# Kernel optimization log

Measured on AMD Instinct MI355X. Metric: run time of the kernel, lower is better.

## Reference

```python
import jax, jax.numpy as jnp
import numpy as np

HEADS, DIM_HEAD, LANDMARKS, PINV_ITERS, RES_K = 8, 64, 256, 6, 33
DIM = 512


def layer_norm(x, w, b, eps=1e-5):
    mu = x.mean(-1, keepdims=True)
    var = ((x - mu) ** 2).mean(-1, keepdims=True)
    return (x - mu) * jax.lax.rsqrt(var + eps) * w + b


def moore_penrose_pinv(x, iters=PINV_ITERS):
    # x: (b, h, m, m)
    abs_x = jnp.abs(x)
    col = abs_x.sum(-1)
    row = abs_x.sum(-2)
    z = jnp.swapaxes(x, -1, -2) / (jnp.max(col) * jnp.max(row))
    I = jnp.eye(x.shape[-1], dtype=x.dtype)
    for _ in range(iters):
        xz = x @ z
        z = 0.25 * z @ (13.0 * I - xz @ (15.0 * I - xz @ (7.0 * I - xz)))
    return z


def nystrom_attention(x, qkv_w, out_w, out_b, res_kernel):
    b, n, _ = x.shape
    h, dh, m = HEADS, DIM_HEAD, LANDMARKS
    l = n // m  # seq chosen divisible by landmarks
    qkv = x @ qkv_w  # (b, n, 3*h*dh)
    q, k, v = jnp.split(qkv, 3, axis=-1)
    def to_heads(t):
        return t.reshape(b, n, h, dh).transpose(0, 2, 1, 3)  # (b,h,n,dh)
    q, k, v = to_heads(q), to_heads(k), to_heads(v)
    q = q * (dh ** -0.5)
    # landmark pooling: mean over contiguous groups of size l
    q_l = q.reshape(b, h, m, l, dh).mean(axis=3)  # (b,h,m,dh)
    k_l = k.reshape(b, h, m, l, dh).mean(axis=3)
    attn1 = jax.nn.softmax(jnp.einsum('bhid,bhjd->bhij', q, k_l), axis=-1)   # (b,h,n,m)
    attn2 = jax.nn.softmax(jnp.einsum('bhid,bhjd->bhij', q_l, k_l), axis=-1) # (b,h,m,m)
    attn3 = jax.nn.softmax(jnp.einsum('bhid,bhjd->bhij', q_l, k), axis=-1)   # (b,h,m,n)
    attn2_inv = moore_penrose_pinv(attn2)
    out = (attn1 @ attn2_inv) @ (attn3 @ v)  # (b,h,n,dh)
    # depthwise residual conv over sequence dim, per head
    pad = (RES_K - 1) // 2
    out = out + jax.lax.conv_general_dilated(
        v, res_kernel, window_strides=(1, 1), padding=((pad, pad), (0, 0)),
        dimension_numbers=('NCHW', 'OIHW', 'NCHW'), feature_group_count=h)
    out = out.transpose(0, 2, 1, 3).reshape(b, n, h * dh)
    return out @ out_w + out_b


def trans_layer(x, p):
    return x + nystrom_attention(layer_norm(x, p['norm_w'], p['norm_b']),
                                 p['qkv_w'], p['out_w'], p['out_b'], p['res_k'])


def setup_inputs() -> dict:
    key = jax.random.key(0)
    ks = jax.random.split(key, 20)
    N, F = 16383, 1024
    d = {}
    d['x'] = jax.random.normal(ks[0], (1, N, F), dtype=jnp.float32)
    d['fc_w'] = jax.random.normal(ks[1], (F, DIM), dtype=jnp.float32) * 0.03
    d['fc_b'] = jnp.zeros((DIM,), dtype=jnp.float32)
    d['cls_token'] = jax.random.normal(ks[2], (1, 1, DIM), dtype=jnp.float32) * 1e-6
    for i, base in [(3, 'l1'), (9, 'l2')]:
        d[base + '_norm_w'] = jnp.ones((DIM,), dtype=jnp.float32)
        d[base + '_norm_b'] = jnp.zeros((DIM,), dtype=jnp.float32)
        d[base + '_qkv_w'] = jax.random.normal(ks[i], (DIM, 3 * DIM), dtype=jnp.float32) * 0.03
        d[base + '_out_w'] = jax.random.normal(ks[i + 1], (DIM, DIM), dtype=jnp.float32) * 0.03
        d[base + '_out_b'] = jnp.zeros((DIM,), dtype=jnp.float32)
        d[base + '_res_k'] = jax.random.normal(ks[i + 2], (HEADS, 1, RES_K, 1), dtype=jnp.float32) * 0.1
    d['norm_w'] = jnp.ones((DIM,), dtype=jnp.float32)
    d['norm_b'] = jnp.zeros((DIM,), dtype=jnp.float32)
    d['clf_w'] = jax.random.normal(ks[15], (DIM, 4), dtype=jnp.float32) * 0.05
    d['clf_b'] = jnp.zeros((4,), dtype=jnp.float32)
    return d


def reference(x, fc_w, fc_b, cls_token, l1_norm_w, l1_norm_b, l1_qkv_w, l1_out_w,
              l1_out_b, l1_res_k, l2_norm_w, l2_norm_b, l2_qkv_w, l2_out_w,
              l2_out_b, l2_res_k, norm_w, norm_b, clf_w, clf_b):
    h = jax.nn.relu(x @ fc_w + fc_b)                       # (1, N, 512)
    h = jnp.concatenate([cls_token, h], axis=1)            # (1, N+1, 512)
    p1 = dict(norm_w=l1_norm_w, norm_b=l1_norm_b, qkv_w=l1_qkv_w,
              out_w=l1_out_w, out_b=l1_out_b, res_k=l1_res_k)
    p2 = dict(norm_w=l2_norm_w, norm_b=l2_norm_b, qkv_w=l2_qkv_w,
              out_w=l2_out_w, out_b=l2_out_b, res_k=l2_res_k)
    h = trans_layer(h, p1)
    h = trans_layer(h, p2)
    h = layer_norm(h, norm_w, norm_b)[:, 0]                # (1, 512)
    logits = h @ clf_w + clf_b                             # (1, n_classes)
    hazards = jax.nn.sigmoid(logits)
    S = jnp.cumprod(1.0 - hazards, axis=1)
    return (hazards, S)
```

## Files before the change

### kernel.cpp

```cpp
#include <hip/hip_runtime.h>

#define NTOK 16384
#define NDIM 512
#define STP_LD 280

typedef __attribute__((ext_vector_type(8))) short short8;
typedef __attribute__((ext_vector_type(4))) float f32x4;

__device__ __forceinline__ unsigned short f2bf(float f) {
  unsigned u = __float_as_uint(f);
  u += 0x7fffu + ((u >> 16) & 1u);
  return (unsigned short)(u >> 16);
}
__device__ __forceinline__ float bf2f(unsigned short u) {
  return __uint_as_float((unsigned)u << 16);
}

__device__ __forceinline__ void gload_lds16(const void* g, void* l) {
  __builtin_amdgcn_global_load_lds(
      (const __attribute__((address_space(1))) unsigned int*)(unsigned long long)(g),
      (__attribute__((address_space(3))) unsigned int*)(unsigned long long)(l), 16, 0, 0);
}

template<int EPI>
__global__ __launch_bounds__(256) void gemm_bf16(
    const unsigned short* __restrict__ A, const unsigned short* __restrict__ Bt,
    float* __restrict__ C, const float* __restrict__ bias,
    int M, int N, int K, int Mstore)
{
  __shared__ unsigned short As[2][128 * 32];
  __shared__ unsigned short Bs[2][128 * 32];
  const int tid = threadIdx.x;
  const int id = blockIdx.y * gridDim.x + blockIdx.x;
  const int nwg8 = (gridDim.x * gridDim.y) >> 3;
  const int logical = (id & 7) * nwg8 + (id >> 3);
  const int row0 = (logical / gridDim.x) * 128;
  const int col0 = (logical % gridDim.x) * 128;
  const int wave = tid >> 6, lane = tid & 63;
  const int wm = (wave >> 1) * 64, wn = (wave & 1) * 64;
  const int quad = lane >> 4, m16 = lane & 15;

  const int r0 = tid >> 2;
  const int c8 = (tid & 3) * 8;
  const unsigned short* Ag0 = A + (size_t)(row0 + r0) * K + c8;
  const unsigned short* Ag1 = A + (size_t)(row0 + r0 + 64) * K + c8;
  const unsigned short* Bg0 = Bt + (size_t)(col0 + r0) * K + c8;
  const unsigned short* Bg1 = Bt + (size_t)(col0 + r0 + 64) * K + c8;
  char* AsB = (char*)As;
  char* BsB = (char*)Bs;
  const int wb = wave * 1024;

  f32x4 acc[4][4] = {};
  const int nc = K >> 5;
  gload_lds16(Ag0, AsB + wb);
  gload_lds16(Ag1, AsB + 4096 + wb);
  gload_lds16(Bg0, BsB + wb);
  gload_lds16(Bg1, BsB + 4096 + wb);
  __syncthreads();
  int b = 0;
  for (int c = 0; c < nc; c++) {
    if (c + 1 < nc) {
      int k1 = (c + 1) * 32;
      gload_lds16(Ag0 + k1, AsB + (b ^ 1) * 8192 + wb);
      gload_lds16(Ag1 + k1, AsB + (b ^ 1) * 8192 + 4096 + wb);
      gload_lds16(Bg0 + k1, BsB + (b ^ 1) * 8192 + wb);
      gload_lds16(Bg1 + k1, BsB + (b ^ 1) * 8192 + 4096 + wb);
    }
    short8 af[4], bf[4];
#pragma unroll
    for (int i = 0; i < 4; i++) {
      af[i] = *(const short8*)&As[b][(wm + i * 16 + m16) * 32 + quad * 8];
      bf[i] = *(const short8*)&Bs[b][(wn + i * 16 + m16) * 32 + quad * 8];
    }
#pragma unroll
    for (int i = 0; i < 4; i++)
#pragma unroll
      for (int j = 0; j < 4; j++)
        acc[i][j] = __builtin_amdgcn_mfma_f32_16x16x32_bf16(af[i], bf[j], acc[i][j], 0, 0, 0);
    __syncthreads();
    b ^= 1;
  }
#pragma unroll
  for (int i = 0; i < 4; i++) {
#pragma unroll
    for (int r = 0; r < 4; r++) {
      int gr = row0 + wm + i * 16 + quad * 4 + r;
      if (gr < Mstore) {
#pragma unroll
        for (int j = 0; j < 4; j++) {
          int gc = col0 + wn + j * 16 + m16;
          float v = acc[i][j][r];
          if (EPI == 1) { v += bias[gc]; v = fmaxf(v, 0.f); }
          if (EPI == 2) { v += bias[gc] + C[(size_t)gr * N + gc]; }
          C[(size_t)gr * N + gc] = v;
        }
      }
    }
  }
}

__global__ __launch_bounds__(256) void qkv_gemm(
    const unsigned short* __restrict__ A, const unsigned short* __restrict__ Bt,
    unsigned short* __restrict__ qb, unsigned short* __restrict__ kb,
    unsigned short* __restrict__ vTb,
    float* __restrict__ q_l, float* __restrict__ k_lT,
    unsigned short* __restrict__ q_lb, unsigned short* __restrict__ k_lb)
{
  __shared__ unsigned short As[2][128 * 32];
  __shared__ unsigned short Bs[2][128 * 32];
  __shared__ unsigned short vt[128 * 136];
  const int tid = threadIdx.x;
  const int id = blockIdx.y * gridDim.x + blockIdx.x;
  const int nwg8 = (gridDim.x * gridDim.y) >> 3;
  const int logical = (id & 7) * nwg8 + (id >> 3);
  const int bx = logical % 12, by = logical / 12;
  const int row0 = by * 128, col0 = bx * 128;
  const int wave = tid >> 6, lane = tid & 63;
  const int wm = (wave >> 1) * 64, wn = (wave & 1) * 64;
  const int quad = lane >> 4, m16 = lane & 15;

  const int r0 = tid >> 2;
  const int c8 = (tid & 3) * 8;
  const unsigned short* Ag0 = A + (size_t)(row0 + r0) * 512 + c8;
  const unsigned short* Ag1 = A + (size_t)(row0 + r0 + 64) * 512 + c8;
  const unsigned short* Bg0 = Bt + (size_t)(col0 + r0) * 512 + c8;
  const unsigned short* Bg1 = Bt + (size_t)(col0 + r0 + 64) * 512 + c8;
  char* AsB = (char*)As;
  char* BsB = (char*)Bs;
  const int wb = wave * 1024;

  f32x4 acc[4][4] = {};
  gload_lds16(Ag0, AsB + wb);
  gload_lds16(Ag1, AsB + 4096 + wb);
  gload_lds16(Bg0, BsB + wb);
  gload_lds16(Bg1, BsB + 4096 + wb);
  __syncthreads();
  int b = 0;
  for (int c = 0; c < 16; c++) {
    if (c < 15) {
      int k1 = (c + 1) * 32;
      gload_lds16(Ag0 + k1, AsB + (b ^ 1) * 8192 + wb);
      gload_lds16(Ag1 + k1, AsB + (b ^ 1) * 8192 + 4096 + wb);
      gload_lds16(Bg0 + k1, BsB + (b ^ 1) * 8192 + wb);
      gload_lds16(Bg1 + k1, BsB + (b ^ 1) * 8192 + 4096 + wb);
    }
    short8 af[4], bf[4];
#pragma unroll
    for (int i = 0; i < 4; i++) {
      af[i] = *(const short8*)&As[b][(wm + i * 16 + m16) * 32 + quad * 8];
      bf[i] = *(const short8*)&Bs[b][(wn + i * 16 + m16) * 32 + quad * 8];
    }
#pragma unroll
    for (int i = 0; i < 4; i++)
#pragma unroll
      for (int j = 0; j < 4; j++)
        acc[i][j] = __builtin_amdgcn_mfma_f32_16x16x32_bf16(af[i], bf[j], acc[i][j], 0, 0, 0);
    __syncthreads();
    b ^= 1;
  }

  const int sel = bx >> 2;
  if (sel == 2) {
#pragma unroll
    for (int i = 0; i < 4; i++)
#pragma unroll
      for (int j = 0; j < 4; j++) {
        int c_l = wn + j * 16 + m16;
        int r_b = wm + i * 16 + quad * 4;
        ushort4 o;
        o.x = f2bf(acc[i][j][0]); o.y = f2bf(acc[i][j][1]);
        o.z = f2bf(acc[i][j][2]); o.w = f2bf(acc[i][j][3]);
        *(ushort4*)&vt[c_l * 136 + r_b] = o;
      }
    __syncthreads();
    const int gc0 = col0 - 1024;
    const int u = tid & 15, cc = tid >> 4;
#pragma unroll
    for (int pass = 0; pass < 8; pass++) {
      int c = pass * 16 + cc;
      short8 v8 = *(const short8*)&vt[c * 136 + u * 8];
      *(short8*)(vTb + (size_t)(gc0 + c) * NTOK + row0 + u * 8) = v8;
    }
  } else {
    const bool isq = (sel == 0);
#pragma unroll
    for (int i = 0; i < 4; i++)
#pragma unroll
      for (int r = 0; r < 4; r++) {
        int gr = row0 + wm + i * 16 + quad * 4 + r;
#pragma unroll
        for (int j = 0; j < 4; j++) {
          int gc = col0 + wn + j * 16 + m16;
          float v = acc[i][j][r];
          if (isq) qb[(size_t)gr * 512 + gc] = f2bf(v * 0.125f);
          else     kb[(size_t)gr * 512 + (gc - 512)] = f2bf(v);
        }
      }
    float ps[4];
#pragma unroll
    for (int j = 0; j < 4; j++) {
      float s = 0.f;
#pragma unroll
      for (int i = 0; i < 4; i++)
#pragma unroll
        for (int r = 0; r < 4; r++) s += acc[i][j][r];
      s += __shfl_xor(s, 16);
      s += __shfl_xor(s, 32);
      ps[j] = s;
    }
    if (quad == 0) {
      const int jg = by * 2 + (wm >> 6);
      const float sc = isq ? (0.125f / 64.f) : (1.f / 64.f);
#pragma unroll
      for (int j = 0; j < 4; j++) {
        int gc = col0 + wn + j * 16 + m16 - (isq ? 0 : 512);
        int hh = gc >> 6, d = gc & 63;
        float p = ps[j] * sc;
        if (isq) {
          size_t o = ((size_t)(hh * 256 + jg)) * 64 + d;
          q_l[o] = p;
          q_lb[o] = f2bf(p);
        } else {
          k_lT[((size_t)hh * 64 + d) * 256 + jg] = p;
          size_t of = ((size_t)hh << 14) + (jg >> 6) * 4096 + (d >> 5) * 2048
                    + ((jg >> 4) & 3) * 512 + ((d >> 3) & 3) * 128 + (jg & 15) * 8 + (d & 7);
          k_lb[of] = f2bf(p);
        }
      }
    }
  }
}

template<bool WN, bool WT, bool WF>
__global__ __launch_bounds__(256) void bmm_pinv64(
    const unsigned short* __restrict__ A, const unsigned short* __restrict__ Bt,
    unsigned short* __restrict__ Cn, unsigned short* __restrict__ Ct,
    float* __restrict__ Cf,
    float an, float bn, float at, float bt)
{
  const int hh = blockIdx.z;
  A  += (size_t)hh << 16;
  Bt += (size_t)hh << 16;
  __shared__ unsigned short As[2][64 * 32];
  __shared__ unsigned short Bs[2][64 * 32];
  const int tid = threadIdx.x;
  const int row0 = blockIdx.y * 64, col0 = blockIdx.x * 64;
  const int wave = tid >> 6, lane = tid & 63;
  const int wm = (wave >> 1) * 32, wn = (wave & 1) * 32;
  const int quad = lane >> 4, m16 = lane & 15;
  const int sr = wave * 16 + (lane >> 2);
  const int sc = (lane & 3) * 8;
  const unsigned short* Ag = A + (size_t)(row0 + sr) * 256 + sc;
  const unsigned short* Bg = Bt + (size_t)(col0 + sr) * 256 + sc;
  char* AsW = (char*)As + wave * 1024;
  char* BsW = (char*)Bs + wave * 1024;

  f32x4 acc[2][2] = {};
  gload_lds16(Ag, AsW);
  gload_lds16(Bg, BsW);
  __syncthreads();
  int b = 0;
  for (int c = 0; c < 8; c++) {
    if (c < 7) {
      gload_lds16(Ag + (c + 1) * 32, AsW + (b ^ 1) * 4096);
      gload_lds16(Bg + (c + 1) * 32, BsW + (b ^ 1) * 4096);
    }
    short8 af[2], bfr[2];
#pragma unroll
    for (int i = 0; i < 2; i++) {
      af[i]  = *(const short8*)&As[b][(wm + i * 16 + m16) * 32 + quad * 8];
      bfr[i] = *(const short8*)&Bs[b][(wn + i * 16 + m16) * 32 + quad * 8];
    }
#pragma unroll
    for (int i = 0; i < 2; i++)
#pragma unroll
      for (int j = 0; j < 2; j++)
        acc[i][j] = __builtin_amdgcn_mfma_f32_16x16x32_bf16(af[i], bfr[j], acc[i][j], 0, 0, 0);
    __syncthreads();
    b ^= 1;
  }
  unsigned short* CnH = Cn + ((size_t)hh << 16);
  unsigned short* CtH = Ct + ((size_t)hh << 16);
  float* CfH = WF ? (Cf + ((size_t)hh << 16)) : nullptr;
#pragma unroll
  for (int i = 0; i < 2; i++) {
#pragma unroll
    for (int r = 0; r < 4; r++) {
      int gr = row0 + wm + i * 16 + quad * 4 + r;
#pragma unroll
      for (int j = 0; j < 2; j++) {
        int gc = col0 + wn + j * 16 + m16;
        float p = acc[i][j][r];
        float diag = (gr == gc) ? 1.f : 0.f;
        if (WN) {
          unsigned short nb_ = f2bf(an * p + bn * diag);
          CnH[(size_t)gr * 256 + gc] = nb_;
          if (WF) CfH[(size_t)gr * 256 + gc] = bf2f(nb_);
        }
        if (WT) CtH[(size_t)gc * 256 + gr] = f2bf(at * p + bt * diag);
      }
    }
  }
}

__global__ void castpad_x(const float* __restrict__ x, unsigned short* __restrict__ xb,
                          size_t nvalid) {
  size_t i4 = ((size_t)blockIdx.x * 256 + threadIdx.x) * 4;
  float4 v = make_float4(0.f, 0.f, 0.f, 0.f);
  if (i4 < nvalid) v = *(const float4*)(x + i4);
  ushort4 o;
  o.x = f2bf(v.x); o.y = f2bf(v.y); o.z = f2bf(v.z); o.w = f2bf(v.w);
  *(ushort4*)(xb + i4) = o;
}

__global__ __launch_bounds__(256) void transpose_cast(
    const float* __restrict__ in, unsigned short* __restrict__ out, int R, int C)
{
  __shared__ float tile[32][33];
  int r0 = blockIdx.x * 32, c0 = blockIdx.y * 32;
  int tx = threadIdx.x & 31, ty = threadIdx.x >> 5;
  for (int yy = ty; yy < 32; yy += 8)
    tile[yy][tx] = in[(size_t)(r0 + yy) * C + c0 + tx];
  __syncthreads();
  for (int yy = ty; yy < 32; yy += 8)
    out[(size_t)(c0 + yy) * R + r0 + tx] = f2bf(tile[tx][yy]);
}

__global__ __launch_bounds__(256) void conv_seq(
    const unsigned short* __restrict__ vTb, const float* __restrict__ res_k,
    unsigned short* __restrict__ convT)
{
  const int c = blockIdx.y;
  const int h = c >> 6;
  const int i0 = (blockIdx.x * 256 + threadIdx.x) * 8;
  float rk[33];
#pragma unroll
  for (int u = 0; u < 33; u++) rk[u] = res_k[h * 33 + u];
  const unsigned short* vr = vTb + (size_t)c * NTOK;
  float win[40];
#pragma unroll
  for (int ch = 0; ch < 5; ch++) {
    int a = i0 - 16 + ch * 8;
    if (a >= 0 && a < NTOK) {
      ushort4 u0 = *(const ushort4*)(vr + a);
      ushort4 u1 = *(const ushort4*)(vr + a + 4);
      win[ch * 8 + 0] = bf2f(u0.x); win[ch * 8 + 1] = bf2f(u0.y);
      win[ch * 8 + 2] = bf2f(u0.z); win[ch * 8 + 3] = bf2f(u0.w);
      win[ch * 8 + 4] = bf2f(u1.x); win[ch * 8 + 5] = bf2f(u1.y);
      win[ch * 8 + 6] = bf2f(u1.z); win[ch * 8 + 7] = bf2f(u1.w);
    } else {
#pragma unroll
      for (int u = 0; u < 8; u++) win[ch * 8 + u] = 0.f;
    }
  }
  ushort4 o0, o1;
  float out[8];
#pragma unroll
  for (int jj = 0; jj < 8; jj++) {
    float s = 0.f;
#pragma unroll
    for (int u = 0; u < 33; u++) s += rk[u] * win[jj + u];
    out[jj] = s;
  }
  o0.x = f2bf(out[0]); o0.y = f2bf(out[1]); o0.z = f2bf(out[2]); o0.w = f2bf(out[3]);
  o1.x = f2bf(out[4]); o1.y = f2bf(out[5]); o1.z = f2bf(out[6]); o1.w = f2bf(out[7]);
  *(ushort4*)(convT + (size_t)c * NTOK + i0) = o0;
  *(ushort4*)(convT + (size_t)c * NTOK + i0 + 4) = o1;
}

template<bool W2>
__global__ __launch_bounds__(256) void bmm_f32(
    const float* __restrict__ A, const float* __restrict__ B, float* __restrict__ C,
    float* __restrict__ C2, int M, int N, int K, float alpha, float beta, float gamma)
{
  const int h = blockIdx.z;
  A += (size_t)h * M * K; B += (size_t)h * K * N;
  size_t cb = (size_t)h * M * N;
  __shared__ float As[16][64];
  __shared__ float Bs[16][64];
  const int tid = threadIdx.x;
  const int row0 = blockIdx.y * 64, col0 = blockIdx.x * 64;
  const int ty = tid >> 4, tx = tid & 15;
  const int ar = tid >> 2, ac = (tid & 3) << 2;
  const int bk = tid >> 4, bj = (tid & 15) << 2;
  float acc[4][4] = {};
  float4 a  = *(const float4*)(A + (size_t)(row0 + ar) * K + ac);
  float4 bv = *(const float4*)(B + (size_t)bk * N + col0 + bj);
  for (int k0 = 0; k0 < K; k0 += 16) {
    As[ac + 0][ar] = a.x; As[ac + 1][ar] = a.y; As[ac + 2][ar] = a.z; As[ac + 3][ar] = a.w;
    *(float4*)&Bs[bk][bj] = bv;
    __syncthreads();
    if (k0 + 16 < K) {
      a  = *(const float4*)(A + (size_t)(row0 + ar) * K + k0 + 16 + ac);
      bv = *(const float4*)(B + (size_t)(k0 + 16 + bk) * N + col0 + bj);
    }
#pragma unroll
    for (int kk = 0; kk < 16; kk++) {
      float4 av = *(float4*)&As[kk][ty << 2];
      float4 bvv = *(float4*)&Bs[kk][tx << 2];
      float a4[4] = {av.x, av.y, av.z, av.w};
      float b4[4] = {bvv.x, bvv.y, bvv.z, bvv.w};
#pragma unroll
      for (int ii = 0; ii < 4; ii++)
#pragma unroll
        for (int jj = 0; jj < 4; jj++) acc[ii][jj] += a4[ii] * b4[jj];
    }
    __syncthreads();
  }
#pragma unroll
  for (int ii = 0; ii < 4; ii++) {
    int gr = row0 + (ty << 2) + ii;
#pragma unroll
    for (int jj = 0; jj < 4; jj++) {
      int gc = col0 + (tx << 2) + jj;
      float diag = (gr == gc) ? 1.f : 0.f;
      float v = alpha * acc[ii][jj] + beta * diag;
      C[cb + (size_t)gr * N + gc] = v;
      if (W2) C2[cb + (size_t)gr * N + gc] = gamma * diag - v;
    }
  }
}

__global__ void cls_copy(const float* __restrict__ cls, float* __restrict__ h) {
  int t = threadIdx.x;
  if (t < 512) h[t] = cls[t];
}

__global__ __launch_bounds__(256) void layernorm_rows(
    const float* __restrict__ x, unsigned short* __restrict__ y,
    const float* __restrict__ w, const float* __restrict__ b)
{
  const int row = blockIdx.x, tid = threadIdx.x;
  const float* xr = x + (size_t)row * NDIM;
  float2 v = ((const float2*)xr)[tid];
  float sum = v.x + v.y, sq = v.x * v.x + v.y * v.y;
#pragma unroll
  for (int off = 32; off; off >>= 1) { sum += __shfl_xor(sum, off); sq += __shfl_xor(sq, off); }
  __shared__ float r1[4], r2[4];
  if ((tid & 63) == 0) { r1[tid >> 6] = sum; r2[tid >> 6] = sq; }
  __syncthreads();
  sum = r1[0] + r1[1] + r1[2] + r1[3];
  sq  = r2[0] + r2[1] + r2[2] + r2[3];
  float mu = sum * (1.f / 512.f);
  float var = sq * (1.f / 512.f) - mu * mu;
  float rs = rsqrtf(var + 1e-5f);
  float a = (v.x - mu) * rs * w[2 * tid]     + b[2 * tid];
  float c = (v.y - mu) * rs * w[2 * tid + 1] + b[2 * tid + 1];
  ((unsigned*)(y + (size_t)row * NDIM))[tid] = (unsigned)f2bf(a) | ((unsigned)f2bf(c) << 16);
}

__global__ __launch_bounds__(256) void attn2_softmax(
    const float* __restrict__ q_l, const float* __restrict__ k_lT,
    float* __restrict__ x2, unsigned short* __restrict__ x2b)
{
  int row = blockIdx.x, h = blockIdx.y, j = threadIdx.x;
  __shared__ float qrow[64];
  __shared__ float red[4];
  if (j < 64) qrow[j] = q_l[(size_t)(h * 256 + row) * 64 + j];
  __syncthreads();
  const float* kt = k_lT + ((size_t)h * 64) * 256 + j;
  float s = 0.f;
#pragma unroll 8
  for (int d = 0; d < 64; d++) s += qrow[d] * kt[(size_t)d * 256];
  float m = s;
#pragma unroll
  for (int off = 32; off; off >>= 1) m = fmaxf(m, __shfl_xor(m, off));
  if ((j & 63) == 0) red[j >> 6] = m;
  __syncthreads();
  m = fmaxf(fmaxf(red[0], red[1]), fmaxf(red[2], red[3]));
  __syncthreads();
  float e = __expf(s - m), l = e;
#pragma unroll
  for (int off = 32; off; off >>= 1) l += __shfl_xor(l, off);
  if ((j & 63) == 0) red[j >> 6] = l;
  __syncthreads();
  l = red[0] + red[1] + red[2] + red[3];
  float val = e / l;
  size_t o = ((size_t)(h * 256 + row) << 8) + j;
  x2[o] = val;
  x2b[o] = f2bf(val);
}

__global__ __launch_bounds__(256) void colrow_max(const float* __restrict__ x2,
                                                  float* __restrict__ scal)
{
  const int h = blockIdx.x, tid = threadIdx.x;
  const float* xh = x2 + ((size_t)h << 16);
  float mx = -1e30f;
  if (blockIdx.y == 0) {
    const int wave = tid >> 6, lane = tid & 63;
    for (int r = wave; r < 256; r += 4) {
      float4 v = *(const float4*)(xh + (size_t)r * 256 + lane * 4);
      float s = v.x + v.y + v.z + v.w;
#pragma unroll
      for (int off = 32; off; off >>= 1) s += __shfl_xor(s, off);
      mx = fmaxf(mx, s);
    }
  } else {
    float cs = 0.f;
    for (int r0 = 0; r0 < 256; r0 += 8) {
      float v[8];
#pragma unroll
      for (int u = 0; u < 8; u++) v[u] = xh[(size_t)(r0 + u) * 256 + tid];
#pragma unroll
      for (int u = 0; u < 8; u++) cs += v[u];
    }
    mx = cs;
  }
#pragma unroll
  for (int off = 32; off; off >>= 1) mx = fmaxf(mx, __shfl_xor(mx, off));
  __shared__ float red[4];
  if ((tid & 63) == 0) red[tid >> 6] = mx;
  __syncthreads();
  if (tid == 0) {
    float m = fmaxf(fmaxf(red[0], red[1]), fmaxf(red[2], red[3]));
    atomicMax((unsigned int*)&scal[blockIdx.y], __float_as_uint(m));
  }
}

__global__ void zinit_bf(const float* __restrict__ x2, unsigned short* __restrict__ zb,
                         unsigned short* __restrict__ zTb, const float* __restrict__ scal)
{
  int idx = blockIdx.x * 256 + threadIdx.x;
  int hh = idx >> 16, i = (idx >> 8) & 255, j = idx & 255;
  float den = scal[0] * scal[1];
  float val = x2[idx] / den;
  unsigned short b = f2bf(val);
  zTb[idx] = b;
  zb[(hh << 16) + (j << 8) + i] = b;
}

__global__ __launch_bounds__(256) void flash_fused(
    const unsigned short* __restrict__ q_lb, const unsigned short* __restrict__ kb,
    const unsigned short* __restrict__ vTb,
    float* __restrict__ Opart, float* __restrict__ mlpart)
{
  const int ks = blockIdx.x, qg = blockIdx.y, h = blockIdx.z;
  const int tid = threadIdx.x;
  const int wave = tid >> 6, lane = tid & 63;
  const int quad = lane >> 4, m16 = lane & 15;

  __shared__ unsigned short Ks[2][4096];
  __shared__ unsigned short Vs[2][4096];
  __shared__ unsigned short pbuf_all[4][16 * 72];
  unsigned short* pbuf = pbuf_all[wave];

  const int key00 = ks * 512;

  const int sr  = (wave << 3) + (lane >> 3);
  const int sxz = (lane & 7) ^ ((lane >> 3) & 7);
  const unsigned short* kst0 = kb + (size_t)(key00 + sr) * 512 + (h << 6) + sxz * 8;
  const unsigned short* kst1 = kst0 + (size_t)32 * 512;
  const unsigned short* vst0 = vTb + (size_t)((h << 6) + sr) * NTOK + key00 + sxz * 8;
  const unsigned short* vst1 = vst0 + (size_t)32 * NTOK;
  char* ldsKw = (char*)&Ks[0][0] + (wave << 10);
  char* ldsVw = (char*)&Vs[0][0] + (wave << 10);

  const int xs  = m16 & 7;
  const int co0 = ((quad) ^ xs) << 3;
  const int co1 = ((4 + quad) ^ xs) << 3;

  const int qrow_w = qg * 64 + wave * 16;
  const unsigned short* qbase = q_lb + ((size_t)h << 14) + (size_t)(qrow_w + m16) * 64;
  short8 aq0 = *(const short8*)(qbase + quad * 8);
  short8 aq1 = *(const short8*)(qbase + 32 + quad * 8);

  float m_e[4], l_e[4];
#pragma unroll
  for (int e = 0; e < 4; e++) { m_e[e] = -1e30f; l_e[e] = 0.f; }
  f32x4 acc_o[4] = {};

#define FF_STAGE(bb, cc) do {                                   \
    size_t ko = (size_t)(cc) * 32768; int vo = (cc) * 64;       \
    gload_lds16(kst0 + ko, ldsKw + (bb) * 8192);                \
    gload_lds16(kst1 + ko, ldsKw + (bb) * 8192 + 4096);         \
    gload_lds16(vst0 + vo, ldsVw + (bb) * 8192);                \
    gload_lds16(vst1 + vo, ldsVw + (bb) * 8192 + 4096);         \
  } while (0)

  FF_STAGE(0, 0);
  __syncthreads();
  int b = 0;
  for (int c = 0; c < 8; c++) {
    if (c < 7) FF_STAGE(b ^ 1, c + 1);
    const unsigned short* Kb = Ks[b];
    const unsigned short* Vb = Vs[b];
    f32x4 s[4] = {};
    __builtin_amdgcn_s_setprio(1);
#pragma unroll
    for (int kt = 0; kt < 4; kt++) {
      const unsigned short* krow = Kb + ((kt << 4) + m16) * 64;
      short8 b0 = *(const short8*)(krow + co0);
      short8 b1 = *(const short8*)(krow + co1);
      s[kt] = __builtin_amdgcn_mfma_f32_16x16x32_bf16(aq0, b0, s[kt], 0, 0, 0);
      s[kt] = __builtin_amdgcn_mfma_f32_16x16x32_bf16(aq1, b1, s[kt], 0, 0, 0);
    }
    __builtin_amdgcn_s_setprio(0);
#pragma unroll
    for (int e = 0; e < 4; e++) {
      float mx = fmaxf(fmaxf(s[0][e], s[1][e]), fmaxf(s[2][e], s[3][e]));
      mx = fmaxf(mx, __shfl_xor(mx, 1));
      mx = fmaxf(mx, __shfl_xor(mx, 2));
      mx = fmaxf(mx, __shfl_xor(mx, 4));
      mx = fmaxf(mx, __shfl_xor(mx, 8));
      float mn = fmaxf(m_e[e], mx);
      float scale = __expf(m_e[e] - mn);
      m_e[e] = mn;
      float sum = 0.f;
#pragma unroll
      for (int kt = 0; kt < 4; kt++) {
        float ev = __expf(s[kt][e] - mn);
        s[kt][e] = ev;
        sum += ev;
      }
      sum += __shfl_xor(sum, 1); sum += __shfl_xor(sum, 2);
      sum += __shfl_xor(sum, 4); sum += __shfl_xor(sum, 8);
      l_e[e] = l_e[e] * scale + sum;
#pragma unroll
      for (int dt = 0; dt < 4; dt++) acc_o[dt][e] *= scale;
    }
#pragma unroll
    for (int kt = 0; kt < 4; kt++)
#pragma unroll
      for (int e = 0; e < 4; e++)
        pbuf[(quad * 4 + e) * 72 + kt * 16 + m16] = f2bf(s[kt][e]);
    asm volatile("s_waitcnt lgkmcnt(0)" ::: "memory");
    short8 ap0 = *(const short8*)&pbuf[m16 * 72 + quad * 8];
    short8 ap1 = *(const short8*)&pbuf[m16 * 72 + 32 + quad * 8];
    __builtin_amdgcn_s_setprio(1);
#pragma unroll
    for (int dt = 0; dt < 4; dt++) {
      const unsigned short* vrow = Vb + ((dt << 4) + m16) * 64;
      short8 bv0 = *(const short8*)(vrow + co0);
      short8 bv1 = *(const short8*)(vrow + co1);
      acc_o[dt] = __builtin_amdgcn_mfma_f32_16x16x32_bf16(ap0, bv0, acc_o[dt], 0, 0, 0);
      acc_o[dt] = __builtin_amdgcn_mfma_f32_16x16x32_bf16(ap1, bv1, acc_o[dt], 0, 0, 0);
    }
    __builtin_amdgcn_s_setprio(0);
    __syncthreads();
    b ^= 1;
  }
#undef FF_STAGE
  float* ob = Opart + ((size_t)(ks * 8 + h) * 256 + qrow_w) * 64;
#pragma unroll
  for (int dt = 0; dt < 4; dt++)
#pragma unroll
    for (int e = 0; e < 4; e++)
      ob[(size_t)(quad * 4 + e) * 64 + dt * 16 + m16] = acc_o[dt][e];
  if (m16 == 0) {
    float* mlb = mlpart + ((size_t)(ks * 8 + h) * 256 + qrow_w) * 2;
#pragma unroll
    for (int e = 0; e < 4; e++) {
      mlb[(quad * 4 + e) * 2]     = m_e[e];
      mlb[(quad * 4 + e) * 2 + 1] = l_e[e];
    }
  }
}

__global__ __launch_bounds__(256) void flash_merge(
    const float* __restrict__ Opart, const float* __restrict__ mlpart,
    float* __restrict__ kv)
{
  const int rc = blockIdx.x, h = blockIdx.y, tid = threadIdx.x;
  const int r = rc * 32 + (tid >> 3);
  const int d0 = (tid & 7) * 8;
  float M = -1e30f;
  for (int ks = 0; ks < 32; ks++)
    M = fmaxf(M, mlpart[((size_t)(ks * 8 + h) * 256 + r) * 2]);
  float L = 0.f;
  float o[8];
#pragma unroll
  for (int j = 0; j < 8; j++) o[j] = 0.f;
  for (int ks = 0; ks < 32; ks++) {
    const float* mlb = mlpart + ((size_t)(ks * 8 + h) * 256 + r) * 2;
    float w = __expf(mlb[0] - M);
    L += mlb[1] * w;
    const float* op = Opart + ((size_t)(ks * 8 + h) * 256 + r) * 64 + d0;
    float4 a = *(const float4*)op;
    float4 b = *(const float4*)(op + 4);
    o[0] += a.x * w; o[1] += a.y * w; o[2] += a.z * w; o[3] += a.w * w;
    o[4] += b.x * w; o[5] += b.y * w; o[6] += b.z * w; o[7] += b.w * w;
  }
  float invL = 1.f / L;
  float* out = kv + ((size_t)(h * 256 + r)) * 64 + d0;
#pragma unroll
  for (int j = 0; j < 8; j++) out[j] = o[j] * invL;
}

__global__ __launch_bounds__(256) void bmt_kernel(
    const float* __restrict__ zf, const float* __restrict__ kv,
    unsigned short* __restrict__ BmT)
{
  const int jb = blockIdx.x, hh = blockIdx.y, tid = threadIdx.x;
  __shared__ float zt[64 * 256];
  const float* zsrc = zf + ((size_t)hh << 16) + (size_t)(jb * 64) * 256;
  for (int rep = 0; rep < 16; rep++) {
    int e4 = (rep * 256 + tid) * 4;
    *(float4*)&zt[e4] = *(const float4*)(zsrc + e4);
  }
  __syncthreads();
  const int d = tid & 63, jg = tid >> 6;
  const float* kvh = kv + ((size_t)hh << 14) + d;
  float acc[16];
#pragma unroll
  for (int u = 0; u < 16; u++) acc[u] = 0.f;
  for (int k0 = 0; k0 < 256; k0 += 8) {
    float kv8[8];
#pragma unroll
    for (int u = 0; u < 8; u++) kv8[u] = kvh[(size_t)(k0 + u) << 6];
#pragma unroll
    for (int jj = 0; jj < 16; jj++) {
      const float* zr = &zt[(jg * 16 + jj) * 256 + k0];
#pragma unroll
      for (int u = 0; u < 8; u++) acc[jj] += zr[u] * kv8[u];
    }
  }
  unsigned short* obh = BmT + ((size_t)hh << 14) + (d >> 5) * 8192
                        + ((d >> 4) & 1) * 512 + (d & 15) * 8;
#pragma unroll
  for (int jj = 0; jj < 16; jj++) {
    int j = jb * 64 + jg * 16 + jj;
    obh[(j >> 5) * 1024 + ((j >> 3) & 3) * 128 + (j & 7)] = f2bf(acc[jj]);
  }
}

__global__ __launch_bounds__(256) void attn1_out(
    const unsigned short* __restrict__ qb, const unsigned short* __restrict__ k_lb,
    const unsigned short* __restrict__ BmT, const unsigned short* __restrict__ convT,
    unsigned short* __restrict__ attn_out)
{
  const int qc = blockIdx.x, h = blockIdx.y, tid = threadIdx.x;
  const int q0 = qc * 32;
  const int wave = tid >> 6, lane = tid & 63;
  const int quad = lane >> 4, m16 = lane & 15;

  __shared__ unsigned short stp[32 * STP_LD];
  __shared__ float redm[4][32], redl[4][32];

  const int mi3 = (wave & 1) * 16;
  const int nbase = (wave >> 1) * 32;
  const int gi0 = q0 + mi3 + quad * 4;
  ushort4 cv4_[2];
#pragma unroll
  for (int t = 0; t < 2; t++) {
    int d = nbase + t * 16 + m16;
    cv4_[t] = *(const ushort4*)(convT + (size_t)((h << 6) + d) * NTOK + gi0);
  }

  f32x4 acc1[2][4] = {};
  {
    const unsigned short* qbase = qb + (size_t)q0 * 512 + (h << 6);
    const unsigned short* kf = k_lb + ((size_t)h << 14) + (wave << 12);
#pragma unroll
    for (int kc = 0; kc < 2; kc++) {
      short8 aq[2], bk[4];
#pragma unroll
      for (int i = 0; i < 2; i++)
        aq[i] = *(const short8*)(qbase + (size_t)(i * 16 + m16) * 512 + kc * 32 + quad * 8);
#pragma unroll
      for (int n = 0; n < 4; n++)
        bk[n] = *(const short8*)(kf + kc * 2048 + n * 512 + lane * 8);
#pragma unroll
      for (int i = 0; i < 2; i++)
#pragma unroll
        for (int n = 0; n < 4; n++)
          acc1[i][n] = __builtin_amdgcn_mfma_f32_16x16x32_bf16(aq[i], bk[n], acc1[i][n], 0, 0, 0);
    }
  }
#pragma unroll
  for (int i = 0; i < 2; i++) {
#pragma unroll
    for (int e = 0; e < 4; e++) {
      float mx = fmaxf(fmaxf(acc1[i][0][e], acc1[i][1][e]), fmaxf(acc1[i][2][e], acc1[i][3][e]));
      mx = fmaxf(mx, __shfl_xor(mx, 1));
      mx = fmaxf(mx, __shfl_xor(mx, 2));
      mx = fmaxf(mx, __shfl_xor(mx, 4));
      mx = fmaxf(mx, __shfl_xor(mx, 8));
      if (m16 == 0) redm[wave][i * 16 + quad * 4 + e] = mx;
    }
  }
  __syncthreads();
#pragma unroll
  for (int i = 0; i < 2; i++) {
#pragma unroll
    for (int e = 0; e < 4; e++) {
      int r = i * 16 + quad * 4 + e;
      float gm = fmaxf(fmaxf(redm[0][r], redm[1][r]), fmaxf(redm[2][r], redm[3][r]));
      float s = 0.f;
#pragma unroll
      for (int n = 0; n < 4; n++) {
        float ev = __expf(acc1[i][n][e] - gm);
        acc1[i][n][e] = ev;
        s += ev;
      }
      s += __shfl_xor(s, 1); s += __shfl_xor(s, 2);
      s += __shfl_xor(s, 4); s += __shfl_xor(s, 8);
      if (m16 == 0) redl[wave][r] = s;
    }
  }
#pragma unroll
  for (int i = 0; i < 2; i++)
#pragma unroll
    for (int n = 0; n < 4; n++) {
      int col = wave * 64 + n * 16 + m16;
#pragma unroll
      for (int e = 0; e < 4; e++)
        stp[(i * 16 + quad * 4 + e) * STP_LD + col] = f2bf(acc1[i][n][e]);
    }
  __syncthreads();

  f32x4 acc3[2] = {};
  {
    const unsigned short* bf_ = BmT + ((size_t)h << 14) + ((nbase >> 5) << 13);
#pragma unroll
    for (int kc = 0; kc < 8; kc++) {
      short8 ap = *(const short8*)&stp[(mi3 + m16) * STP_LD + kc * 32 + quad * 8];
#pragma unroll
      for (int t = 0; t < 2; t++) {
        short8 bp = *(const short8*)(bf_ + kc * 1024 + t * 512 + lane * 8);
        acc3[t] = __builtin_amdgcn_mfma_f32_16x16x32_bf16(ap, bp, acc3[t], 0, 0, 0);
      }
    }
  }
#pragma unroll
  for (int t = 0; t < 2; t++) {
    int d = nbase + t * 16 + m16;
    unsigned short cvs[4] = {cv4_[t].x, cv4_[t].y, cv4_[t].z, cv4_[t].w};
#pragma unroll
    for (int e = 0; e < 4; e++) {
      int lr = mi3 + quad * 4 + e;
      float l = redl[0][lr] + redl[1][lr] + redl[2][lr] + redl[3][lr];
      float v = acc3[t][e] / l + bf2f(cvs[e]);
      attn_out[((size_t)(gi0 + e) << 9) + (h << 6) + d] = f2bf(v);
    }
  }
}

__global__ __launch_bounds__(256) void final_head(
    const float* __restrict__ hrow, const float* __restrict__ nw, const float* __restrict__ nb,
    const float* __restrict__ cw, const float* __restrict__ cb, float* __restrict__ out)
{
  const int tid = threadIdx.x;
  __shared__ float ln0[512];
  __shared__ float r1[4], r2[4];
  __shared__ float lg[4][4];
  float2 v = ((const float2*)hrow)[tid];
  float sum = v.x + v.y, sq = v.x * v.x + v.y * v.y;
#pragma unroll
  for (int off = 32; off; off >>= 1) { sum += __shfl_xor(sum, off); sq += __shfl_xor(sq, off); }
  if ((tid & 63) == 0) { r1[tid >> 6] = sum; r2[tid >> 6] = sq; }
  __syncthreads();
  sum = r1[0] + r1[1] + r1[2] + r1[3];
  sq  = r2[0] + r2[1] + r2[2] + r2[3];
  float mu = sum * (1.f / 512.f);
  float var = sq * (1.f / 512.f) - mu * mu;
  float rs = rsqrtf(var + 1e-5f);
  ln0[2 * tid]     = (v.x - mu) * rs * nw[2 * tid]     + nb[2 * tid];
  ln0[2 * tid + 1] = (v.y - mu) * rs * nw[2 * tid + 1] + nb[2 * tid + 1];
  __syncthreads();
  float p[4] = {0.f, 0.f, 0.f, 0.f};
  for (int k = tid; k < 512; k += 256) {
    float lv = ln0[k];
#pragma unroll
    for (int c = 0; c < 4; c++) p[c] += lv * cw[k * 4 + c];
  }
#pragma unroll
  for (int off = 32; off; off >>= 1)
#pragma unroll
    for (int c = 0; c < 4; c++) p[c] += __shfl_xor(p[c], off);
  if ((tid & 63) == 0) {
    int w = tid >> 6;
#pragma unroll
    for (int c = 0; c < 4; c++) lg[w][c] = p[c];
  }
  __syncthreads();
  if (tid == 0) {
    float cum = 1.f;
    for (int c = 0; c < 4; c++) {
      float logit = lg[0][c] + lg[1][c] + lg[2][c] + lg[3][c] + cb[c];
      float hz = 1.f / (1.f + __expf(-logit));
      out[c] = hz;
      cum *= (1.f - hz);
      out[4 + c] = cum;
    }
  }
}

extern "C" void kernel_launch(void* const* d_in, const int* in_sizes, int n_in,
                              void* d_out, int out_size, void* d_ws, size_t ws_size,
                              hipStream_t stream)
{
  (void)in_sizes; (void)n_in; (void)out_size; (void)ws_size;
  const float* x    = (const float*)d_in[0];
  const float* fc_w = (const float*)d_in[1];
  const float* fc_b = (const float*)d_in[2];
  const float* cls  = (const float*)d_in[3];
  const float* nw[2]   = {(const float*)d_in[4],  (const float*)d_in[10]};
  const float* nb[2]   = {(const float*)d_in[5],  (const float*)d_in[11]};
  const float* qkvw[2] = {(const float*)d_in[6],  (const float*)d_in[12]};
  const float* outw[2] = {(const float*)d_in[7],  (const float*)d_in[13]};
  const float* outb[2] = {(const float*)d_in[8],  (const float*)d_in[14]};
  const float* resk[2] = {(const float*)d_in[9],  (const float*)d_in[15]};
  const float* fnw = (const float*)d_in[16];
  const float* fnb = (const float*)d_in[17];
  const float* cw  = (const float*)d_in[18];
  const float* cb  = (const float*)d_in[19];

  float* ws = (float*)d_ws;
  float* h    = ws; ws += (size_t)NTOK * NDIM;
  float* qkv  = ws; ws += (size_t)NTOK * 1536;
  float* bigv = ws; ws += (size_t)(512 * NTOK) / 2;
  float* q_l  = ws; ws += 8 * 256 * 64;
  float* k_lT = ws; ws += 8 * 256 * 64;
  float* x2   = ws; ws += 8 * 256 * 256;
  float* zf   = ws; ws += 8 * 256 * 256;
  float* zfin = ws; ws += 8 * 256 * 256;
  float* tA   = ws; ws += 8 * 256 * 256;
  float* tB   = ws; ws += 8 * 256 * 256;
  float* tC   = ws; ws += 8 * 256 * 256;
  float* kv   = ws; ws += 8 * 256 * 64;
  float* scal = ws; ws += 64;
  unsigned short* actb = (unsigned short*)ws; ws += (size_t)NTOK * NDIM / 2;
  unsigned short* wT   = (unsigned short*)ws; ws += (1536 * 512) / 2;
  unsigned short* qb   = (unsigned short*)ws; ws += (size_t)NTOK * NDIM / 2;
  unsigned short* k_lb = (unsigned short*)ws; ws += (8 * 256 * 64) / 2;
  unsigned short* q_lb = (unsigned short*)ws; ws += (8 * 256 * 64) / 2;
  unsigned short* x2b  = (unsigned short*)ws; ws += (8 * 256 * 256) / 2;
  unsigned short* zb0  = (unsigned short*)ws; ws += (8 * 256 * 256) / 2;
  unsigned short* zb1  = (unsigned short*)ws; ws += (8 * 256 * 256) / 2;
  unsigned short* zT0  = (unsigned short*)ws; ws += (8 * 256 * 256) / 2;
  unsigned short* zT1  = (unsigned short*)ws; ws += (8 * 256 * 256) / 2;
  unsigned short* xzb  = (unsigned short*)ws; ws += (8 * 256 * 256) / 2;
  unsigned short* t1T  = (unsigned short*)ws; ws += (8 * 256 * 256) / 2;
  unsigned short* t2T  = (unsigned short*)ws; ws += (8 * 256 * 256) / 2;
  unsigned short* t3T  = (unsigned short*)ws; ws += (8 * 256 * 256) / 2;
  unsigned short* BmT  = (unsigned short*)ws; ws += (8 * 64 * 256) / 2;
  unsigned short* kbuf = (unsigned short*)ws; ws += (size_t)NTOK * NDIM / 2;

  unsigned short* xb  = (unsigned short*)qkv;
  unsigned short* vTb = (unsigned short*)bigv;
  float* Opart  = qkv;
  float* mlpart = qkv + (size_t)32 * 8 * 256 * 64;
  unsigned short* convT = (unsigned short*)(qkv + (size_t)32 * 8 * 256 * 64 + 32 * 8 * 256 * 2);

  unsigned short* zbp[2] = {zb0, zb1};
  unsigned short* zTp[2] = {zT0, zT1};

  castpad_x<<<16384, 256, 0, stream>>>(x, xb, (size_t)16383 * 1024);
  transpose_cast<<<dim3(32, 16), 256, 0, stream>>>(fc_w, wT, 1024, 512);
  gemm_bf16<1><<<dim3(4, 128), 256, 0, stream>>>(xb, wT, h + 512, fc_b,
                                                 16384, 512, 1024, 16383);
  cls_copy<<<1, 512, 0, stream>>>(cls, h);

  for (int L = 0; L < 2; L++) {
    layernorm_rows<<<NTOK, 256, 0, stream>>>(h, actb, nw[L], nb[L]);
    transpose_cast<<<dim3(16, 48), 256, 0, stream>>>(qkvw[L], wT, 512, 1536);
    qkv_gemm<<<dim3(12, 128), 256, 0, stream>>>(actb, wT, qb, kbuf, vTb,
                                                q_l, k_lT, q_lb, k_lb);
    attn2_softmax<<<dim3(256, 8), 256, 0, stream>>>(q_l, k_lT, x2, x2b);
    hipMemsetAsync(scal, 0, 2 * sizeof(float), stream);
    colrow_max<<<dim3(8, 2), 256, 0, stream>>>(x2, scal);
    zinit_bf<<<2048, 256, 0, stream>>>(x2, zbp[0], zTp[0], scal);

    flash_fused<<<dim3(32, 4, 8), 256, 0, stream>>>(q_lb, kbuf, vTb, Opart, mlpart);
    flash_merge<<<dim3(8, 8), 256, 0, stream>>>(Opart, mlpart, kv);
    conv_seq<<<dim3(8, 512), 256, 0, stream>>>(vTb, resk[L], convT);

    int cur = 0;
    dim3 pg(4, 4, 8);
    for (int it = 0; it < 5; it++) {
      bmm_pinv64<true,  true, false><<<pg, 256, 0, stream>>>(x2b, zTp[cur], xzb, t1T, nullptr,
                                                             1.f, 0.f, -1.f, 7.f);
      bmm_pinv64<false, true, false><<<pg, 256, 0, stream>>>(xzb, t1T, nullptr, t2T, nullptr,
                                                             0.f, 0.f, -1.f, 15.f);
      bmm_pinv64<false, true, false><<<pg, 256, 0, stream>>>(xzb, t2T, nullptr, t3T, nullptr,
                                                             0.f, 0.f, -1.f, 13.f);
      if (it < 4)
        bmm_pinv64<true, true, false><<<pg, 256, 0, stream>>>(zbp[cur], t3T, zbp[cur ^ 1],
                                                              zTp[cur ^ 1], nullptr,
                                                              0.25f, 0.f, 0.25f, 0.f);
      else
        bmm_pinv64<true, true, true><<<pg, 256, 0, stream>>>(zbp[cur], t3T, zbp[cur ^ 1],
                                                             zTp[cur ^ 1], zf,
                                                             0.25f, 0.f, 0.25f, 0.f);
      cur ^= 1;
    }
    bmm_f32<true ><<<dim3(4, 4, 8), 256, 0, stream>>>(x2, zf, tA, tB, 256, 256, 256, 1.f, 0.f, 7.f);
    bmm_f32<false><<<dim3(4, 4, 8), 256, 0, stream>>>(tA, tB, tC, nullptr, 256, 256, 256, -1.f, 15.f, 0.f);
    bmm_f32<false><<<dim3(4, 4, 8), 256, 0, stream>>>(tA, tC, tB, nullptr, 256, 256, 256, -1.f, 13.f, 0.f);
    bmm_f32<false><<<dim3(4, 4, 8), 256, 0, stream>>>(zf, tB, zfin, nullptr, 256, 256, 256, 0.25f, 0.f, 0.f);

    bmt_kernel<<<dim3(4, 8), 256, 0, stream>>>(zfin, kv, BmT);
    attn1_out<<<dim3(512, 8), 256, 0, stream>>>(qb, k_lb, BmT, convT, actb);
    transpose_cast<<<dim3(16, 16), 256, 0, stream>>>(outw[L], wT, 512, 512);
    gemm_bf16<2><<<dim3(4, 128), 256, 0, stream>>>(actb, wT, h, outb[L],
                                                   NTOK, 512, 512, NTOK);
  }
  final_head<<<1, 256, 0, stream>>>(h, fnw, fnb, cw, cb, (float*)d_out);
}
```

Baseline: 951.1 us.

## Stage QKV epilogue through aliased LDS and drop the memset and cls launches

The q/k epilogue of qkv_gemm now writes bf16 results into a shared-memory tile and stores rows back as coalesced 16-byte vectors, replacing scattered 2-byte global stores. The staging tile is aliased onto the double-buffered A/B operand buffers, which shrinks the LDS footprint and may allow more resident workgroups. The cls row copy is folded into castpad_x. The atomicMax with its preceding memset is replaced by per-block partial maxima that zinit_bf reduces, removing two small launches per layer. This adds a block barrier in the epilogue and requires scal to hold 16 floats.

```diff
diff --git a/kernel.cpp b/kernel.cpp
--- a/kernel.cpp
+++ b/kernel.cpp
@@ -106,9 +106,10 @@
     float* __restrict__ q_l, float* __restrict__ k_lT,
     unsigned short* __restrict__ q_lb, unsigned short* __restrict__ k_lb)
 {
-  __shared__ unsigned short As[2][128 * 32];
-  __shared__ unsigned short Bs[2][128 * 32];
-  __shared__ unsigned short vt[128 * 136];
+  __shared__ unsigned short smem[17408];
+  unsigned short* AsU = smem;
+  unsigned short* BsU = smem + 8192;
+  unsigned short* vt  = smem;
   const int tid = threadIdx.x;
   const int id = blockIdx.y * gridDim.x + blockIdx.x;
   const int nwg8 = (gridDim.x * gridDim.y) >> 3;
@@ -125,8 +126,8 @@
   const unsigned short* Ag1 = A + (size_t)(row0 + r0 + 64) * 512 + c8;
   const unsigned short* Bg0 = Bt + (size_t)(col0 + r0) * 512 + c8;
   const unsigned short* Bg1 = Bt + (size_t)(col0 + r0 + 64) * 512 + c8;
-  char* AsB = (char*)As;
-  char* BsB = (char*)Bs;
+  char* AsB = (char*)AsU;
+  char* BsB = (char*)BsU;
   const int wb = wave * 1024;
 
   f32x4 acc[4][4] = {};
@@ -147,8 +148,8 @@
     short8 af[4], bf[4];
 #pragma unroll
     for (int i = 0; i < 4; i++) {
-      af[i] = *(const short8*)&As[b][(wm + i * 16 + m16) * 32 + quad * 8];
-      bf[i] = *(const short8*)&Bs[b][(wn + i * 16 + m16) * 32 + quad * 8];
+      af[i] = *(const short8*)&AsU[b * 4096 + (wm + i * 16 + m16) * 32 + quad * 8];
+      bf[i] = *(const short8*)&BsU[b * 4096 + (wn + i * 16 + m16) * 32 + quad * 8];
     }
 #pragma unroll
     for (int i = 0; i < 4; i++)
@@ -183,17 +184,16 @@
     }
   } else {
     const bool isq = (sel == 0);
+    const float mul = isq ? 0.125f : 1.f;
 #pragma unroll
     for (int i = 0; i < 4; i++)
 #pragma unroll
-      for (int r = 0; r < 4; r++) {
-        int gr = row0 + wm + i * 16 + quad * 4 + r;
-#pragma unroll
-        for (int j = 0; j < 4; j++) {
-          int gc = col0 + wn + j * 16 + m16;
-          float v = acc[i][j][r];
-          if (isq) qb[(size_t)gr * 512 + gc] = f2bf(v * 0.125f);
-          else     kb[(size_t)gr * 512 + (gc - 512)] = f2bf(v);
+      for (int j = 0; j < 4; j++) {
+        int lc = wn + j * 16 + m16;
+#pragma unroll
+        for (int r = 0; r < 4; r++) {
+          int lr = wm + i * 16 + quad * 4 + r;
+          vt[lr * 136 + lc] = f2bf(acc[i][j][r] * mul);
         }
       }
     float ps[4];
@@ -227,6 +227,16 @@
           k_lb[of] = f2bf(p);
         }
       }
+    }
+    __syncthreads();
+    unsigned short* ob = isq ? (qb + (size_t)row0 * 512 + col0)
+                             : (kb + (size_t)row0 * 512 + (col0 - 512));
+    const int u = tid & 15, cc = tid >> 4;
+#pragma unroll
+    for (int pass = 0; pass < 8; pass++) {
+      int rloc = pass * 16 + cc;
+      short8 v8 = *(const short8*)&vt[rloc * 136 + u * 8];
+      *(short8*)(ob + (size_t)rloc * 512 + u * 8) = v8;
     }
   }
 }
@@ -304,13 +314,16 @@
 }
 
 __global__ void castpad_x(const float* __restrict__ x, unsigned short* __restrict__ xb,
-                          size_t nvalid) {
+                          size_t nvalid, const float* __restrict__ cls,
+                          float* __restrict__ h) {
   size_t i4 = ((size_t)blockIdx.x * 256 + threadIdx.x) * 4;
   float4 v = make_float4(0.f, 0.f, 0.f, 0.f);
   if (i4 < nvalid) v = *(const float4*)(x + i4);
   ushort4 o;
   o.x = f2bf(v.x); o.y = f2bf(v.y); o.z = f2bf(v.z); o.w = f2bf(v.w);
   *(ushort4*)(xb + i4) = o;
+  if (blockIdx.x == 0 && threadIdx.x < 128)
+    *(float4*)(h + threadIdx.x * 4) = *(const float4*)(cls + threadIdx.x * 4);
 }
 
 __global__ __launch_bounds__(256) void transpose_cast(
@@ -421,11 +434,6 @@
   }
 }
 
-__global__ void cls_copy(const float* __restrict__ cls, float* __restrict__ h) {
-  int t = threadIdx.x;
-  if (t < 512) h[t] = cls[t];
-}
-
 __global__ __launch_bounds__(256) void layernorm_rows(
     const float* __restrict__ x, unsigned short* __restrict__ y,
     const float* __restrict__ w, const float* __restrict__ b)
@@ -512,10 +520,8 @@
   __shared__ float red[4];
   if ((tid & 63) == 0) red[tid >> 6] = mx;
   __syncthreads();
-  if (tid == 0) {
-    float m = fmaxf(fmaxf(red[0], red[1]), fmaxf(red[2], red[3]));
-    atomicMax((unsigned int*)&scal[blockIdx.y], __float_as_uint(m));
-  }
+  if (tid == 0)
+    scal[blockIdx.y * 8 + h] = fmaxf(fmaxf(red[0], red[1]), fmaxf(red[2], red[3]));
 }
 
 __global__ void zinit_bf(const float* __restrict__ x2, unsigned short* __restrict__ zb,
@@ -523,7 +529,10 @@
 {
   int idx = blockIdx.x * 256 + threadIdx.x;
   int hh = idx >> 16, i = (idx >> 8) & 255, j = idx & 255;
-  float den = scal[0] * scal[1];
+  float m0 = scal[0], m1 = scal[8];
+#pragma unroll
+  for (int u = 1; u < 8; u++) { m0 = fmaxf(m0, scal[u]); m1 = fmaxf(m1, scal[8 + u]); }
+  float den = m0 * m1;
   float val = x2[idx] / den;
   unsigned short b = f2bf(val);
   zTb[idx] = b;
@@ -946,11 +955,10 @@
   unsigned short* zbp[2] = {zb0, zb1};
   unsigned short* zTp[2] = {zT0, zT1};
 
-  castpad_x<<<16384, 256, 0, stream>>>(x, xb, (size_t)16383 * 1024);
+  castpad_x<<<16384, 256, 0, stream>>>(x, xb, (size_t)16383 * 1024, cls, h);
   transpose_cast<<<dim3(32, 16), 256, 0, stream>>>(fc_w, wT, 1024, 512);
   gemm_bf16<1><<<dim3(4, 128), 256, 0, stream>>>(xb, wT, h + 512, fc_b,
                                                  16384, 512, 1024, 16383);
-  cls_copy<<<1, 512, 0, stream>>>(cls, h);
 
   for (int L = 0; L < 2; L++) {
     layernorm_rows<<<NTOK, 256, 0, stream>>>(h, actb, nw[L], nb[L]);
@@ -958,7 +966,6 @@
     qkv_gemm<<<dim3(12, 128), 256, 0, stream>>>(actb, wT, qb, kbuf, vTb,
                                                 q_l, k_lT, q_lb, k_lb);
     attn2_softmax<<<dim3(256, 8), 256, 0, stream>>>(q_l, k_lT, x2, x2b);
-    hipMemsetAsync(scal, 0, 2 * sizeof(float), stream);
     colrow_max<<<dim3(8, 2), 256, 0, stream>>>(x2, scal);
     zinit_bf<<<2048, 256, 0, stream>>>(x2, zbp[0], zTp[0], scal);
 
@@ -994,7 +1001,7 @@
     attn1_out<<<dim3(512, 8), 256, 0, stream>>>(qb, k_lb, BmT, convT, actb);
     transpose_cast<<<dim3(16, 16), 256, 0, stream>>>(outw[L], wT, 512, 512);
     gemm_bf16<2><<<dim3(4, 128), 256, 0, stream>>>(actb, wT, h, outb[L],
-                                                   NTOK, 512, 512, NTOK);
+                                                   16384, 512, 512, NTOK);
   }
   final_head<<<1, 256, 0, stream>>>(h, fnw, fnb, cw, cb, (float*)d_out);
 }
```

Result: faster. 930.8 us (-2.1%).
